# Kernel optimization log

Measured on AMD Instinct MI355X. Metric: run time of the kernel, lower is better.

The kernel has to match this reference:

```python
import jax, jax.numpy as jnp
import numpy as np
from jax import lax

# Per-tensor power-of-two scales (ScalingImplType.CONST / POWER_OF_TWO in Brevitas)
S_ACT8 = 2.0 ** -4   # 8-bit signed input quant scale
S_ACT4 = 2.0 ** -1   # 4-bit signed input quant scale
S_W = 2.0 ** -2      # per-tensor weight quant scale
S_RELU = 2.0 ** -2   # 4-bit unsigned QuantReLU scale


def fq(x, scale, qmin, qmax):
    # fake-quant with straight-through estimator (STE)
    q = jnp.clip(jnp.round(x / scale), qmin, qmax) * scale
    return x + lax.stop_gradient(q - x)


def fq_signed(x, scale, bits):
    return fq(x, scale, -(2 ** (bits - 1)), 2 ** (bits - 1) - 1)


def fq_uint(x, scale, bits):
    return fq(x, scale, 0, 2 ** bits - 1)


def qconv(x, w, in_bits, w_bits, s_in, stride=1, padding=0, groups=1):
    xq = fq_signed(x, s_in, in_bits)
    wq = fq_signed(w, S_W, w_bits)
    return lax.conv_general_dilated(
        xq, wq, (stride, stride), [(padding, padding)] * 2,
        feature_group_count=groups,
        dimension_numbers=('NCHW', 'OIHW', 'NCHW'))


def maxpool(x, k, s):
    return lax.reduce_window(x, -jnp.inf, lax.max,
                             (1, 1, k, k), (1, 1, s, s), 'VALID')


def dwsep(x, dw, pw):
    c = x.shape[1]
    x = qconv(x, dw, 4, 4, S_ACT4, padding=1, groups=c)  # depthwise 3x3
    x = qconv(x, pw, 4, 4, S_ACT4)                       # pointwise 1x1
    return x


def qrelu4(x):
    return fq_uint(jax.nn.relu(x), S_RELU, 4)


def setup_inputs() -> dict:
    key = jax.random.key(0)
    ks = jax.random.split(key, 10)
    B = 1024
    mk = lambda k, shp, sc=0.5: jax.random.normal(k, shp, jnp.float32) * sc
    return {
        'x': jax.random.normal(ks[0], (B, 3, 32, 32), jnp.float32),
        'w0': mk(ks[1], (3, 3, 1, 1)),
        'dw1': mk(ks[2], (3, 1, 3, 3)),
        'pw1': mk(ks[3], (32, 3, 1, 1)),
        'dw2': mk(ks[4], (32, 1, 3, 3)),
        'pw2': mk(ks[5], (64, 32, 1, 1)),
        'dw3': mk(ks[6], (64, 1, 3, 3)),
        'pw3': mk(ks[7], (128, 64, 1, 1)),
        'wc1': mk(ks[8], (256, 128, 1, 1)),
        'wc2': mk(ks[9], (10, 256, 1, 1)),
    }


def reference(x, w0, dw1, pw1, dw2, pw2, dw3, pw3, wc1, wc2):
    # features
    h = qconv(x, w0, 8, 8, S_ACT8)            # 1x1, 3->3, 8-bit
    h = dwsep(h, dw1, pw1)                    # 3->32, 32x32
    h = qrelu4(h)
    h = maxpool(h, 2, 2)                      # 16x16
    h = dwsep(h, dw2, pw2)                    # 32->64
    h = qrelu4(h)
    h = maxpool(h, 2, 2)                      # 8x8
    h = dwsep(h, dw3, pw3)                    # 64->128
    h = qrelu4(h)
    h = maxpool(h, 8, 1)                      # 1x1
    # classifier
    h = qconv(h, wc1, 4, 4, S_ACT4)           # 128->256
    h = qrelu4(h)
    h = qconv(h, wc2, 4, 4, S_ACT4)           # 256->10
    h = fq_signed(h, S_ACT8, 8)               # output quant int8
    return h
```

## Files before the change

kernel.cpp:

```cpp
#include <hip/hip_runtime.h>

typedef int v4i __attribute__((ext_vector_type(4)));

#define W0i   0
#define DW1i  9
#define PW1i  36
#define DW2i  132
#define DW3i  420
#define PW2p  996
#define PW3p  1508
#define WC1p  3556
#define WC2p  11748
#define PW2Fb 12388
#define PW3Fb 12900
#define DW2pk 14948
#define DW3pk 15092
#define WTOT  15380

__device__ __forceinline__ int iclamp(int v, int lo, int hi) {
  return v < lo ? lo : (v > hi ? hi : v);
}
__device__ __forceinline__ int rne4(int a) {
  return (a + 1 + ((a >> 2) & 1)) >> 2;
}
__device__ __forceinline__ int rne32(int a) {
  return (a + 15 + ((a >> 5) & 1)) >> 5;
}

__device__ __forceinline__ int dot4(int a, int b, int c) {
#if defined(__has_builtin) && __has_builtin(__builtin_amdgcn_sdot4)
  return __builtin_amdgcn_sdot4(a, b, c, false);
#else
  c += ((a << 24) >> 24) * ((b << 24) >> 24);
  c += ((a << 16) >> 24) * ((b << 16) >> 24);
  c += ((a <<  8) >> 24) * ((b <<  8) >> 24);
  c += (a >> 24) * (b >> 24);
  return c;
#endif
}

__device__ __forceinline__ int alignb(int hi, int lo, int sh) {
#if defined(__has_builtin) && __has_builtin(__builtin_amdgcn_alignbyte)
  return __builtin_amdgcn_alignbyte(hi, lo, sh);
#else
  return (int)(((((unsigned long long)(unsigned)hi) << 32) |
                (unsigned)lo) >> (8 * sh));
#endif
}

__device__ __forceinline__ int pack3(int a, int b, int c) {
  return (a & 0xff) | ((b & 0xff) << 8) | ((c & 0xff) << 16);
}

__device__ __forceinline__ int pk_mad16(int a, int b, int c) {
  int d;
  asm("v_pk_mad_i16 %0, %1, %2, %3" : "=v"(d) : "v"(a), "v"(b), "v"(c));
  return d;
}
__device__ __forceinline__ int pk_add16(int a, int b) {
  int d;
  asm("v_pk_add_i16 %0, %1, %2" : "=v"(d) : "v"(a), "v"(b));
  return d;
}
__device__ __forceinline__ int pk_ashr16(int sh, int a) {
  int d;
  asm("v_pk_ashrrev_i16 %0, %1, %2" : "=v"(d) : "v"(sh), "v"(a));
  return d;
}
__device__ __forceinline__ int pk_max16(int a, int b) {
  int d;
  asm("v_pk_max_i16 %0, %1, %2" : "=v"(d) : "v"(a), "v"(b));
  return d;
}
__device__ __forceinline__ int pk_min16(int a, int b) {
  int d;
  asm("v_pk_min_i16 %0, %1, %2" : "=v"(d) : "v"(a), "v"(b));
  return d;
}
__device__ __forceinline__ int rne4s_pk(int a) {
  const int sh = 0x00020002, one = 0x00010001;
  int t = pk_ashr16(sh, a);
  t &= one;
  t += one;
  int s4 = pk_add16(a, t);
  int r = pk_ashr16(sh, s4);
  r = pk_max16(r, (int)0xFFF8FFF8);
  r = pk_min16(r, 0x00070007);
  return r;
}

__device__ __forceinline__ int max4(v4i d) {
  int a = d[0] > d[1] ? d[0] : d[1];
  int b = d[2] > d[3] ? d[2] : d[3];
  return a > b ? a : b;
}

__global__ __launch_bounds__(256) void prep_weights(
    const float* __restrict__ w0,  const float* __restrict__ dw1,
    const float* __restrict__ pw1, const float* __restrict__ dw2,
    const float* __restrict__ pw2, const float* __restrict__ dw3,
    const float* __restrict__ pw3, const float* __restrict__ wc1,
    const float* __restrict__ wc2, int* __restrict__ ws) {
  int t = blockIdx.x * blockDim.x + threadIdx.x;
  if (t >= WTOT) return;
  if (t < PW2p) {
    float w; int lo = -8, hi = 7;
    if (t < DW1i)      { w = w0[t];        lo = -128; hi = 127; }
    else if (t < PW1i)   w = dw1[t - DW1i];
    else if (t < DW2i)   w = pw1[t - PW1i];
    else if (t < DW3i)   w = dw2[t - DW2i];
    else                 w = dw3[t - DW3i];
    ws[t] = iclamp((int)rintf(w * 4.f), lo, hi);
  } else if (t < PW2Fb) {
    const float* src;
    if (t < WC1p) {
      if (t < PW3p) src = pw2 + (t - PW2p) * 4;
      else          src = pw3 + (t - PW3p) * 4;
    } else {
      if (t < WC2p) src = wc1 + (t - WC1p) * 4;
      else          src = wc2 + (t - WC2p) * 4;
    }
    int p = 0;
#pragma unroll
    for (int b = 0; b < 4; b++) {
      int c = iclamp((int)rintf(src[b] * 4.f), -8, 7);
      p |= (c & 0xff) << (8 * b);
    }
    ws[t] = p;
  } else if (t < PW3Fb) {
    int i = t - PW2Fb;
    int nt = i >> 7, r = i & 127, lane = r >> 1, dw = r & 1;
    int n = nt * 16 + (lane & 15);
    int kb = (lane >> 4) * 8 + dw * 4;
    int p = 0;
#pragma unroll
    for (int b = 0; b < 4; b++) {
      int c = iclamp((int)rintf(pw2[n * 32 + kb + b] * 4.f), -8, 7);
      p |= (c & 0xff) << (8 * b);
    }
    ws[t] = p;
  } else if (t < DW2pk) {
    int i = t - PW3Fb;
    int g = i >> 7, r = i & 127, lane = r >> 1, dw = r & 1;
    int nt = g >> 1, kh = g & 1;
    int n = nt * 16 + (lane & 15);
    int kb = kh * 32 + (lane >> 4) * 8 + dw * 4;
    int p = 0;
#pragma unroll
    for (int b = 0; b < 4; b++) {
      int c = iclamp((int)rintf(pw3[n * 64 + kb + b] * 4.f), -8, 7);
      p |= (c & 0xff) << (8 * b);
    }
    ws[t] = p;
  } else if (t < DW3pk) {
    int i = t - DW2pk;
    int cq = i / 18, r = i - cq * 18, t9 = r >> 1, par = r & 1;
    int wl = iclamp((int)rintf(dw2[(cq * 4 + par) * 9 + t9] * 4.f), -8, 7);
    int wh = iclamp((int)rintf(dw2[(cq * 4 + 2 + par) * 9 + t9] * 4.f), -8, 7);
    ws[t] = (wl & 0xFFFF) | (wh << 16);
  } else {
    int i = t - DW3pk;
    int cq = i / 18, r = i - cq * 18, t9 = r >> 1, par = r & 1;
    int wl = iclamp((int)rintf(dw3[(cq * 4 + par) * 9 + t9] * 4.f), -8, 7);
    int wh = iclamp((int)rintf(dw3[(cq * 4 + 2 + par) * 9 + t9] * 4.f), -8, 7);
    ws[t] = (wl & 0xFFFF) | (wh << 16);
  }
}

__global__ __launch_bounds__(256, 4) void fused_net(
    const float* __restrict__ x,
    const int*   __restrict__ wq,
    float* __restrict__ out)
{
  const int img = blockIdx.x;
  const int tid = threadIdx.x;

  __shared__ __align__(16) int bufAi[2560];
  __shared__ __align__(16) int bufBi[2592];
  __shared__ int s_red[256];

  {
    const float* xim = x + (size_t)img * 3072;
    const int p4 = tid * 4;
    float4 v0 = *(const float4*)(xim + p4);
    float4 v1 = *(const float4*)(xim + 1024 + p4);
    float4 v2 = *(const float4*)(xim + 2048 + p4);
    int w[9];
#pragma unroll
    for (int i = 0; i < 9; i++) w[i] = wq[W0i + i];
#define Q8(v) iclamp((int)rintf((v) * 16.f), -128, 127)
    int a0[4] = {Q8(v0.x), Q8(v0.y), Q8(v0.z), Q8(v0.w)};
    int a1[4] = {Q8(v1.x), Q8(v1.y), Q8(v1.z), Q8(v1.w)};
    int a2[4] = {Q8(v2.x), Q8(v2.y), Q8(v2.z), Q8(v2.w)};
#undef Q8
#pragma unroll
    for (int o = 0; o < 3; o++) {
      int pk = 0;
#pragma unroll
      for (int j = 0; j < 4; j++) {
        int s = a0[j] * w[o * 3] + a1[j] * w[o * 3 + 1] + a2[j] * w[o * 3 + 2];
        pk |= (iclamp(rne32(s), -8, 7) & 0xff) << (8 * j);
      }
      bufAi[o * 256 + tid] = pk;
    }
  }
  __syncthreads();

  {
    const int y = tid >> 3, q = tid & 7;
#pragma unroll
    for (int c = 0; c < 3; c++) {
      int wr[3];
#pragma unroll
      for (int r = 0; r < 3; r++)
        wr[r] = pack3(wq[DW1i + c * 9 + r * 3], wq[DW1i + c * 9 + r * 3 + 1],
                      wq[DW1i + c * 9 + r * 3 + 2]);
      const int* ap = bufAi + c * 256;
      int acc0 = 0, acc1 = 0, acc2 = 0, acc3 = 0;
#pragma unroll
      for (int ky = 0; ky < 3; ky++) {
        int yy = y + ky - 1;
        if (yy < 0 || yy > 31) continue;
        int base = yy * 8 + q;
        int dC = ap[base];
        int dL = q ? ap[base - 1] : 0;
        int dR = (q < 7) ? ap[base + 1] : 0;
        int w = wr[ky];
        acc0 = dot4(alignb(dC, dL, 3), w, acc0);
        acc1 = dot4(dC, w, acc1);
        acc2 = dot4(alignb(dR, dC, 1), w, acc2);
        acc3 = dot4(alignb(dR, dC, 2), w, acc3);
      }
      int pk = (iclamp(rne4(acc0), -8, 7) & 0xff) |
               ((iclamp(rne4(acc1), -8, 7) & 0xff) << 8) |
               ((iclamp(rne4(acc2), -8, 7) & 0xff) << 16) |
               ((iclamp(rne4(acc3), -8, 7) & 0xff) << 24);
      bufBi[c * 256 + tid] = pk;
    }
  }
  __syncthreads();

  {
    const int py = tid >> 4, px = tid & 15;
    const unsigned char* bB = (const unsigned char*)bufBi;
    unsigned u[3][2];
#pragma unroll
    for (int c = 0; c < 3; c++)
#pragma unroll
      for (int dy = 0; dy < 2; dy++)
        u[c][dy] = *(const unsigned short*)(bB + c * 1024 +
                                            (2 * py + dy) * 32 + 2 * px);
    int a[4];
#pragma unroll
    for (int d = 0; d < 4; d++) {
      int dy = d >> 1, dx = d & 1;
      unsigned t1 = __builtin_amdgcn_perm(u[1][dy], u[0][dy],
                                          0x0C0C0000u | ((4 + dx) << 8) | dx);
      a[d] = (int)__builtin_amdgcn_perm(u[2][dy], t1,
                                        0x0C000100u | ((4 + dx) << 16));
    }
#pragma unroll
    for (int it = 0; it < 8; it++) {
      int pk = 0;
#pragma unroll
      for (int j = 0; j < 4; j++) {
        int o = it * 4 + j;
        int wpk = pack3(wq[PW1i + o * 3], wq[PW1i + o * 3 + 1],
                        wq[PW1i + o * 3 + 2]);
        int m0 = dot4(a[0], wpk, 0), m1 = dot4(a[1], wpk, 0);
        int m2 = dot4(a[2], wpk, 0), m3 = dot4(a[3], wpk, 0);
        int mx = max(max(m0, m1), max(m2, m3));
        pk |= iclamp(rne4(mx), 0, 7) << (8 * j);
      }
      bufAi[py * 149 + px * 9 + it] = pk;
    }
  }
  __syncthreads();

  for (int it2 = 0; it2 < 2; it2++) {
    int idx = tid + 256 * it2;
    int cq = __builtin_amdgcn_readfirstlane(idx >> 6);
    int s = idx & 63;
    int y = s >> 2, x0 = (s & 3) << 2;
    int we[9], wo[9];
    {
      const int2* wp = (const int2*)(wq + DW2pk + cq * 18);
#pragma unroll
      for (int t9 = 0; t9 < 9; t9++) { int2 v = wp[t9]; we[t9] = v.x; wo[t9] = v.y; }
    }
    int acce[4] = {}, acco[4] = {};
#pragma unroll
    for (int ky = 0; ky < 3; ky++) {
      int yy = y + ky - 1;
      if (yy < 0 || yy > 15) continue;
      int rb = yy * 149 + cq;
      int rd[6];
      rd[0] = (x0 > 0) ? bufAi[rb + (x0 - 1) * 9] : 0;
      rd[1] = bufAi[rb + x0 * 9];
      rd[2] = bufAi[rb + (x0 + 1) * 9];
      rd[3] = bufAi[rb + (x0 + 2) * 9];
      rd[4] = bufAi[rb + (x0 + 3) * 9];
      rd[5] = (x0 < 12) ? bufAi[rb + (x0 + 4) * 9] : 0;
      int ee[6], eo[6];
#pragma unroll
      for (int k = 0; k < 6; k++) {
        ee[k] = rd[k] & 0x000F000F;
        eo[k] = (rd[k] >> 8) & 0x000F000F;
      }
#pragma unroll
      for (int j = 0; j < 4; j++)
#pragma unroll
        for (int kx = 0; kx < 3; kx++) {
          acce[j] = pk_mad16(ee[j + kx], we[ky * 3 + kx], acce[j]);
          acco[j] = pk_mad16(eo[j + kx], wo[ky * 3 + kx], acco[j]);
        }
    }
#pragma unroll
    for (int j = 0; j < 4; j++) {
      int re = rne4s_pk(acce[j]);
      int ro = rne4s_pk(acco[j]);
      bufBi[y * 162 + (x0 + j) * 10 + cq] =
          (re & 0x00FF00FF) | ((ro & 0x00FF00FF) << 8);
    }
  }
  __syncthreads();

#pragma unroll
  for (int i = 0; i < 4; i++) {
    int id = tid + 256 * i;
    int m = id >> 2, c2 = id & 3;
    int qp = m >> 2, d = m & 3;
    int sy = ((qp >> 3) << 1) + (d >> 1);
    int sx = ((qp & 7) << 1) + (d & 1);
    long v = *(const long*)(bufBi + sy * 162 + sx * 10 + c2 * 2);
    *(long*)(bufAi + m * 10 + c2 * 2) = v;
  }
  __syncthreads();

  {
    const int w = tid >> 6, lane = tid & 63;
    const int lm = lane & 15, kg = lane >> 4;
    const int ntp = (w & 1) * 2;
    const int mtb = (w >> 1) * 8;
    const long bw0 = *(const long*)(wq + PW2Fb + (ntp * 64 + lane) * 2);
    const long bw1 = *(const long*)(wq + PW2Fb + ((ntp + 1) * 64 + lane) * 2);
    const signed char* Ab = (const signed char*)bufAi;
    signed char* A2c = (signed char*)bufBi;
    const int n0 = ntp * 16 + lm, n1 = (ntp + 1) * 16 + lm;
#pragma unroll 4
    for (int mt = mtb; mt < mtb + 8; mt++) {
      int m = mt * 16 + lm;
      long av = *(const long*)(Ab + m * 40 + kg * 8);
      v4i d0 = __builtin_amdgcn_mfma_i32_16x16x32_i8(av, bw0, (v4i){0, 0, 0, 0},
                                                     0, 0, 0);
      v4i d1 = __builtin_amdgcn_mfma_i32_16x16x32_i8(av, bw1, (v4i){0, 0, 0, 0},
                                                     0, 0, 0);
      int qp = mt * 4 + kg;
      int py = qp >> 3, px = qp & 7;
      int bb = (py * 137 + px * 17) * 4;
      A2c[bb + n0] = (signed char)iclamp(rne4(max4(d0)), 0, 7);
      A2c[bb + n1] = (signed char)iclamp(rne4(max4(d1)), 0, 7);
    }
  }
  __syncthreads();

  {
    int cq2 = tid >> 4;
    int s = tid & 15;
    int y = s >> 1, x0 = (s & 1) << 2;
    int we[9], wo[9];
    {
      const int2* wp = (const int2*)(wq + DW3pk + cq2 * 18);
#pragma unroll
      for (int t9 = 0; t9 < 9; t9++) { int2 v = wp[t9]; we[t9] = v.x; wo[t9] = v.y; }
    }
    int acce[4] = {}, acco[4] = {};
#pragma unroll
    for (int ky = 0; ky < 3; ky++) {
      int yy = y + ky - 1;
      if (yy < 0 || yy > 7) continue;
      int rb = yy * 137 + cq2;
      int rd[6];
      rd[0] = (x0 == 4) ? bufBi[rb + (x0 - 1) * 17] : 0;
      rd[1] = bufBi[rb + x0 * 17];
      rd[2] = bufBi[rb + (x0 + 1) * 17];
      rd[3] = bufBi[rb + (x0 + 2) * 17];
      rd[4] = bufBi[rb + (x0 + 3) * 17];
      rd[5] = (x0 == 0) ? bufBi[rb + (x0 + 4) * 17] : 0;
      int ee[6], eo[6];
#pragma unroll
      for (int k = 0; k < 6; k++) {
        ee[k] = rd[k] & 0x000F000F;
        eo[k] = (rd[k] >> 8) & 0x000F000F;
      }
#pragma unroll
      for (int j = 0; j < 4; j++)
#pragma unroll
        for (int kx = 0; kx < 3; kx++) {
          acce[j] = pk_mad16(ee[j + kx], we[ky * 3 + kx], acce[j]);
          acco[j] = pk_mad16(eo[j + kx], wo[ky * 3 + kx], acco[j]);
        }
    }
#pragma unroll
    for (int j = 0; j < 4; j++) {
      int re = rne4s_pk(acce[j]);
      int ro = rne4s_pk(acco[j]);
      bufAi[(y * 8 + x0 + j) * 18 + cq2] =
          (re & 0x00FF00FF) | ((ro & 0x00FF00FF) << 8);
    }
  }
  __syncthreads();

  {
    const int w = tid >> 6, lane = tid & 63;
    const int lm = lane & 15, kg = lane >> 4;
    const signed char* Ab = (const signed char*)bufAi;
    signed char* fcin = (signed char*)bufBi;
    long b0v[2], b1v[2];
#pragma unroll
    for (int h = 0; h < 2; h++) {
      int nt = w * 2 + h;
      b0v[h] = *(const long*)(wq + PW3Fb + (nt * 2 + 0) * 128 + lane * 2);
      b1v[h] = *(const long*)(wq + PW3Fb + (nt * 2 + 1) * 128 + lane * 2);
    }
    int mx[2] = {-1000000, -1000000};
#pragma unroll
    for (int mt = 0; mt < 4; mt++) {
      int m = mt * 16 + lm;
      long a0 = *(const long*)(Ab + m * 72 + kg * 8);
      long a1 = *(const long*)(Ab + m * 72 + 32 + kg * 8);
#pragma unroll
      for (int h = 0; h < 2; h++) {
        v4i d = __builtin_amdgcn_mfma_i32_16x16x32_i8(a0, b0v[h],
                                                      (v4i){0, 0, 0, 0}, 0, 0, 0);
        d = __builtin_amdgcn_mfma_i32_16x16x32_i8(a1, b1v[h], d, 0, 0, 0);
        int t4 = max4(d);
        mx[h] = mx[h] > t4 ? mx[h] : t4;
      }
    }
#pragma unroll
    for (int h = 0; h < 2; h++) {
      int red = max(mx[h], __shfl_xor(mx[h], 16));
      red = max(red, __shfl_xor(red, 32));
      if (lane < 16)
        fcin[(w * 2 + h) * 16 + lm] = (signed char)iclamp(rne4(red), 0, 7);
    }
  }
  __syncthreads();

  {
    const int4* wp = (const int4*)(wq + WC1p + tid * 32);
    const int4* mp = (const int4*)bufBi;
    int acc = 0;
#pragma unroll
    for (int rI = 0; rI < 8; rI++) {
      int4 a = mp[rI]; int4 w = wp[rI];
      acc = dot4(a.x, w.x, acc); acc = dot4(a.y, w.y, acc);
      acc = dot4(a.z, w.z, acc); acc = dot4(a.w, w.w, acc);
    }
    ((signed char*)bufAi)[tid] = (signed char)iclamp(rne4(acc), 0, 7);
  }
  __syncthreads();

  if (tid < 80) {
    int k = tid >> 3, j = tid & 7;
    const int4* wp = (const int4*)(wq + WC2p + k * 64 + j * 8);
    int4 w0v = wp[0], w1v = wp[1];
    const int4* ap = (const int4*)bufAi;
    int4 A0 = ap[j * 2], A1 = ap[j * 2 + 1];
    int acc = dot4(A0.x, w0v.x, 0);
    acc = dot4(A0.y, w0v.y, acc); acc = dot4(A0.z, w0v.z, acc);
    acc = dot4(A0.w, w0v.w, acc);
    acc = dot4(A1.x, w1v.x, acc); acc = dot4(A1.y, w1v.y, acc);
    acc = dot4(A1.z, w1v.z, acc); acc = dot4(A1.w, w1v.w, acc);
    s_red[tid] = acc;
  }
  __syncthreads();
  if (tid < 10) {
    int acc = 0;
#pragma unroll
    for (int j = 0; j < 8; j++) acc += s_red[tid * 8 + j];
    int code = iclamp(2 * acc, -128, 127);
    out[(size_t)img * 10 + tid] = (float)code * 0.0625f;
  }
}

extern "C" void kernel_launch(void* const* d_in, const int* in_sizes, int n_in,
                              void* d_out, int out_size, void* d_ws, size_t ws_size,
                              hipStream_t stream) {
  const float* x   = (const float*)d_in[0];
  const float* w0  = (const float*)d_in[1];
  const float* dw1 = (const float*)d_in[2];
  const float* pw1 = (const float*)d_in[3];
  const float* dw2 = (const float*)d_in[4];
  const float* pw2 = (const float*)d_in[5];
  const float* dw3 = (const float*)d_in[6];
  const float* pw3 = (const float*)d_in[7];
  const float* wc1 = (const float*)d_in[8];
  const float* wc2 = (const float*)d_in[9];
  int*   wsq = (int*)d_ws;
  float* out = (float*)d_out;

  prep_weights<<<(WTOT + 255) / 256, 256, 0, stream>>>(
      w0, dw1, pw1, dw2, pw2, dw3, pw3, wc1, wc2, wsq);
  fused_net<<<1024, 256, 0, stream>>>(x, wsq, out);
}
```

Baseline: 95.97 us.

## Double block size to 512 threads and redistribute per-stage work

Raises the fused per-image kernel from 256 to 512 threads and splits every stage's work across the larger block: two pixels per thread at the input, finer task splits for the depthwise and pointwise stages, and one MFMA tile per wave for pw2/pw3. It also drops the separate repack pass after the second depthwise conv by writing directly into the swizzled layout the MFMA stage reads, which removes one barrier and one LDS copy. The aim is more parallel work per image and fewer serial loop steps. The cost is higher register pressure from the 512-thread launch bounds and idle threads in the small classifier stages.

```diff
diff --git a/kernel.cpp b/kernel.cpp
--- a/kernel.cpp
+++ b/kernel.cpp
@@ -167,7 +167,7 @@
   }
 }
 
-__global__ __launch_bounds__(256, 4) void fused_net(
+__global__ __launch_bounds__(512, 8) void fused_net(
     const float* __restrict__ x,
     const int*   __restrict__ wq,
     float* __restrict__ out)
@@ -181,67 +181,65 @@
 
   {
     const float* xim = x + (size_t)img * 3072;
-    const int p4 = tid * 4;
-    float4 v0 = *(const float4*)(xim + p4);
-    float4 v1 = *(const float4*)(xim + 1024 + p4);
-    float4 v2 = *(const float4*)(xim + 2048 + p4);
+    const int p2 = tid * 2;
+    float2 v0 = *(const float2*)(xim + p2);
+    float2 v1 = *(const float2*)(xim + 1024 + p2);
+    float2 v2 = *(const float2*)(xim + 2048 + p2);
     int w[9];
 #pragma unroll
     for (int i = 0; i < 9; i++) w[i] = wq[W0i + i];
 #define Q8(v) iclamp((int)rintf((v) * 16.f), -128, 127)
-    int a0[4] = {Q8(v0.x), Q8(v0.y), Q8(v0.z), Q8(v0.w)};
-    int a1[4] = {Q8(v1.x), Q8(v1.y), Q8(v1.z), Q8(v1.w)};
-    int a2[4] = {Q8(v2.x), Q8(v2.y), Q8(v2.z), Q8(v2.w)};
+    int a0[2] = {Q8(v0.x), Q8(v0.y)};
+    int a1[2] = {Q8(v1.x), Q8(v1.y)};
+    int a2[2] = {Q8(v2.x), Q8(v2.y)};
 #undef Q8
 #pragma unroll
     for (int o = 0; o < 3; o++) {
-      int pk = 0;
-#pragma unroll
-      for (int j = 0; j < 4; j++) {
-        int s = a0[j] * w[o * 3] + a1[j] * w[o * 3 + 1] + a2[j] * w[o * 3 + 2];
-        pk |= (iclamp(rne32(s), -8, 7) & 0xff) << (8 * j);
-      }
-      bufAi[o * 256 + tid] = pk;
-    }
+      int c0 = iclamp(rne32(a0[0] * w[o * 3] + a1[0] * w[o * 3 + 1] +
+                            a2[0] * w[o * 3 + 2]), -8, 7);
+      int c1 = iclamp(rne32(a0[1] * w[o * 3] + a1[1] * w[o * 3 + 1] +
+                            a2[1] * w[o * 3 + 2]), -8, 7);
+      ((short*)bufAi)[o * 512 + tid] =
+          (short)((c0 & 0xff) | ((c1 & 0xff) << 8));
+    }
+  }
+  __syncthreads();
+
+  for (int task = tid; task < 768; task += 512) {
+    int c = task >> 8, pos = task & 255;
+    int y = pos >> 3, q = pos & 7;
+    int wr[3];
+#pragma unroll
+    for (int r = 0; r < 3; r++)
+      wr[r] = pack3(wq[DW1i + c * 9 + r * 3], wq[DW1i + c * 9 + r * 3 + 1],
+                    wq[DW1i + c * 9 + r * 3 + 2]);
+    const int* ap = bufAi + c * 256;
+    int acc0 = 0, acc1 = 0, acc2 = 0, acc3 = 0;
+#pragma unroll
+    for (int ky = 0; ky < 3; ky++) {
+      int yy = y + ky - 1;
+      if (yy < 0 || yy > 31) continue;
+      int base = yy * 8 + q;
+      int dC = ap[base];
+      int dL = q ? ap[base - 1] : 0;
+      int dR = (q < 7) ? ap[base + 1] : 0;
+      int w = wr[ky];
+      acc0 = dot4(alignb(dC, dL, 3), w, acc0);
+      acc1 = dot4(dC, w, acc1);
+      acc2 = dot4(alignb(dR, dC, 1), w, acc2);
+      acc3 = dot4(alignb(dR, dC, 2), w, acc3);
+    }
+    int pk = (iclamp(rne4(acc0), -8, 7) & 0xff) |
+             ((iclamp(rne4(acc1), -8, 7) & 0xff) << 8) |
+             ((iclamp(rne4(acc2), -8, 7) & 0xff) << 16) |
+             ((iclamp(rne4(acc3), -8, 7) & 0xff) << 24);
+    bufBi[c * 256 + pos] = pk;
   }
   __syncthreads();
 
   {
-    const int y = tid >> 3, q = tid & 7;
-#pragma unroll
-    for (int c = 0; c < 3; c++) {
-      int wr[3];
-#pragma unroll
-      for (int r = 0; r < 3; r++)
-        wr[r] = pack3(wq[DW1i + c * 9 + r * 3], wq[DW1i + c * 9 + r * 3 + 1],
-                      wq[DW1i + c * 9 + r * 3 + 2]);
-      const int* ap = bufAi + c * 256;
-      int acc0 = 0, acc1 = 0, acc2 = 0, acc3 = 0;
-#pragma unroll
-      for (int ky = 0; ky < 3; ky++) {
-        int yy = y + ky - 1;
-        if (yy < 0 || yy > 31) continue;
-        int base = yy * 8 + q;
-        int dC = ap[base];
-        int dL = q ? ap[base - 1] : 0;
-        int dR = (q < 7) ? ap[base + 1] : 0;
-        int w = wr[ky];
-        acc0 = dot4(alignb(dC, dL, 3), w, acc0);
-        acc1 = dot4(dC, w, acc1);
-        acc2 = dot4(alignb(dR, dC, 1), w, acc2);
-        acc3 = dot4(alignb(dR, dC, 2), w, acc3);
-      }
-      int pk = (iclamp(rne4(acc0), -8, 7) & 0xff) |
-               ((iclamp(rne4(acc1), -8, 7) & 0xff) << 8) |
-               ((iclamp(rne4(acc2), -8, 7) & 0xff) << 16) |
-               ((iclamp(rne4(acc3), -8, 7) & 0xff) << 24);
-      bufBi[c * 256 + tid] = pk;
-    }
-  }
-  __syncthreads();
-
-  {
-    const int py = tid >> 4, px = tid & 15;
+    const int p = tid >> 1, itb = (tid & 1) * 4;
+    const int py = p >> 4, px = p & 15;
     const unsigned char* bB = (const unsigned char*)bufBi;
     unsigned u[3][2];
 #pragma unroll
@@ -260,7 +258,7 @@
                                         0x0C000100u | ((4 + dx) << 16));
     }
 #pragma unroll
-    for (int it = 0; it < 8; it++) {
+    for (int it = itb; it < itb + 4; it++) {
       int pk = 0;
 #pragma unroll
       for (int j = 0; j < 4; j++) {
@@ -277,10 +275,9 @@
   }
   __syncthreads();
 
-  for (int it2 = 0; it2 < 2; it2++) {
-    int idx = tid + 256 * it2;
-    int cq = __builtin_amdgcn_readfirstlane(idx >> 6);
-    int s = idx & 63;
+  {
+    int cq = __builtin_amdgcn_readfirstlane(tid >> 6);
+    int s = tid & 63;
     int y = s >> 2, x0 = (s & 3) << 2;
     int we[9], wo[9];
     {
@@ -315,142 +312,102 @@
           acco[j] = pk_mad16(eo[j + kx], wo[ky * 3 + kx], acco[j]);
         }
     }
+    const int py = y >> 1, dy = y & 1;
 #pragma unroll
     for (int j = 0; j < 4; j++) {
+      int xx = x0 + j;
+      int qp = py * 8 + (xx >> 1);
+      int q = qp ^ (py & 3);
+      int m = q * 4 + dy * 2 + (xx & 1);
       int re = rne4s_pk(acce[j]);
       int ro = rne4s_pk(acco[j]);
-      bufBi[y * 162 + (x0 + j) * 10 + cq] =
-          (re & 0x00FF00FF) | ((ro & 0x00FF00FF) << 8);
-    }
-  }
-  __syncthreads();
-
-#pragma unroll
-  for (int i = 0; i < 4; i++) {
-    int id = tid + 256 * i;
-    int m = id >> 2, c2 = id & 3;
-    int qp = m >> 2, d = m & 3;
-    int sy = ((qp >> 3) << 1) + (d >> 1);
-    int sx = ((qp & 7) << 1) + (d & 1);
-    long v = *(const long*)(bufBi + sy * 162 + sx * 10 + c2 * 2);
-    *(long*)(bufAi + m * 10 + c2 * 2) = v;
+      bufBi[m * 10 + cq] = (re & 0x00FF00FF) | ((ro & 0x00FF00FF) << 8);
+    }
   }
   __syncthreads();
 
   {
     const int w = tid >> 6, lane = tid & 63;
     const int lm = lane & 15, kg = lane >> 4;
-    const int ntp = (w & 1) * 2;
-    const int mtb = (w >> 1) * 8;
-    const long bw0 = *(const long*)(wq + PW2Fb + (ntp * 64 + lane) * 2);
-    const long bw1 = *(const long*)(wq + PW2Fb + ((ntp + 1) * 64 + lane) * 2);
-    const signed char* Ab = (const signed char*)bufAi;
-    signed char* A2c = (signed char*)bufBi;
-    const int n0 = ntp * 16 + lm, n1 = (ntp + 1) * 16 + lm;
+    const int nt = w & 3, mtb = (w >> 2) * 8;
+    const long bw = *(const long*)(wq + PW2Fb + (nt * 64 + lane) * 2);
+    const signed char* Ab = (const signed char*)bufBi;
+    signed char* A2c = (signed char*)bufAi;
+    const int n = nt * 16 + lm;
 #pragma unroll 4
     for (int mt = mtb; mt < mtb + 8; mt++) {
       int m = mt * 16 + lm;
       long av = *(const long*)(Ab + m * 40 + kg * 8);
-      v4i d0 = __builtin_amdgcn_mfma_i32_16x16x32_i8(av, bw0, (v4i){0, 0, 0, 0},
+      v4i d0 = __builtin_amdgcn_mfma_i32_16x16x32_i8(av, bw, (v4i){0, 0, 0, 0},
                                                      0, 0, 0);
-      v4i d1 = __builtin_amdgcn_mfma_i32_16x16x32_i8(av, bw1, (v4i){0, 0, 0, 0},
-                                                     0, 0, 0);
-      int qp = mt * 4 + kg;
+      int q = mt * 4 + kg;
+      int qp = q ^ ((q >> 3) & 3);
       int py = qp >> 3, px = qp & 7;
-      int bb = (py * 137 + px * 17) * 4;
-      A2c[bb + n0] = (signed char)iclamp(rne4(max4(d0)), 0, 7);
-      A2c[bb + n1] = (signed char)iclamp(rne4(max4(d1)), 0, 7);
-    }
-  }
-  __syncthreads();
-
-  {
-    int cq2 = tid >> 4;
-    int s = tid & 15;
-    int y = s >> 1, x0 = (s & 1) << 2;
+      A2c[(py * 137 + px * 17) * 4 + n] =
+          (signed char)iclamp(rne4(max4(d0)), 0, 7);
+    }
+  }
+  __syncthreads();
+
+  for (int it = 0; it < 2; it++) {
+    int cq2 = __builtin_amdgcn_readfirstlane(tid >> 6) * 2 + it;
+    int pos = tid & 63;
+    int y = pos >> 3, xx = pos & 7;
     int we[9], wo[9];
     {
       const int2* wp = (const int2*)(wq + DW3pk + cq2 * 18);
 #pragma unroll
       for (int t9 = 0; t9 < 9; t9++) { int2 v = wp[t9]; we[t9] = v.x; wo[t9] = v.y; }
     }
-    int acce[4] = {}, acco[4] = {};
+    int acce = 0, acco = 0;
 #pragma unroll
     for (int ky = 0; ky < 3; ky++) {
       int yy = y + ky - 1;
       if (yy < 0 || yy > 7) continue;
-      int rb = yy * 137 + cq2;
-      int rd[6];
-      rd[0] = (x0 == 4) ? bufBi[rb + (x0 - 1) * 17] : 0;
-      rd[1] = bufBi[rb + x0 * 17];
-      rd[2] = bufBi[rb + (x0 + 1) * 17];
-      rd[3] = bufBi[rb + (x0 + 2) * 17];
-      rd[4] = bufBi[rb + (x0 + 3) * 17];
-      rd[5] = (x0 == 0) ? bufBi[rb + (x0 + 4) * 17] : 0;
-      int ee[6], eo[6];
-#pragma unroll
-      for (int k = 0; k < 6; k++) {
-        ee[k] = rd[k] & 0x000F000F;
-        eo[k] = (rd[k] >> 8) & 0x000F000F;
+#pragma unroll
+      for (int kx = 0; kx < 3; kx++) {
+        int x2 = xx + kx - 1;
+        if (x2 < 0 || x2 > 7) continue;
+        int rdv = bufAi[yy * 137 + x2 * 17 + cq2];
+        int ee = rdv & 0x000F000F, eo = (rdv >> 8) & 0x000F000F;
+        acce = pk_mad16(ee, we[ky * 3 + kx], acce);
+        acco = pk_mad16(eo, wo[ky * 3 + kx], acco);
       }
-#pragma unroll
-      for (int j = 0; j < 4; j++)
-#pragma unroll
-        for (int kx = 0; kx < 3; kx++) {
-          acce[j] = pk_mad16(ee[j + kx], we[ky * 3 + kx], acce[j]);
-          acco[j] = pk_mad16(eo[j + kx], wo[ky * 3 + kx], acco[j]);
-        }
-    }
-#pragma unroll
-    for (int j = 0; j < 4; j++) {
-      int re = rne4s_pk(acce[j]);
-      int ro = rne4s_pk(acco[j]);
-      bufAi[(y * 8 + x0 + j) * 18 + cq2] =
-          (re & 0x00FF00FF) | ((ro & 0x00FF00FF) << 8);
-    }
+    }
+    int re = rne4s_pk(acce), ro = rne4s_pk(acco);
+    bufBi[pos * 18 + cq2] = (re & 0x00FF00FF) | ((ro & 0x00FF00FF) << 8);
   }
   __syncthreads();
 
   {
-    const int w = tid >> 6, lane = tid & 63;
+    const int nt = tid >> 6, lane = tid & 63;
     const int lm = lane & 15, kg = lane >> 4;
-    const signed char* Ab = (const signed char*)bufAi;
-    signed char* fcin = (signed char*)bufBi;
-    long b0v[2], b1v[2];
-#pragma unroll
-    for (int h = 0; h < 2; h++) {
-      int nt = w * 2 + h;
-      b0v[h] = *(const long*)(wq + PW3Fb + (nt * 2 + 0) * 128 + lane * 2);
-      b1v[h] = *(const long*)(wq + PW3Fb + (nt * 2 + 1) * 128 + lane * 2);
-    }
-    int mx[2] = {-1000000, -1000000};
+    const signed char* Ab = (const signed char*)bufBi;
+    signed char* fcin = (signed char*)bufAi;
+    const long b0 = *(const long*)(wq + PW3Fb + (nt * 2 + 0) * 128 + lane * 2);
+    const long b1 = *(const long*)(wq + PW3Fb + (nt * 2 + 1) * 128 + lane * 2);
+    int mx = -1000000;
 #pragma unroll
     for (int mt = 0; mt < 4; mt++) {
       int m = mt * 16 + lm;
       long a0 = *(const long*)(Ab + m * 72 + kg * 8);
       long a1 = *(const long*)(Ab + m * 72 + 32 + kg * 8);
-#pragma unroll
-      for (int h = 0; h < 2; h++) {
-        v4i d = __builtin_amdgcn_mfma_i32_16x16x32_i8(a0, b0v[h],
-                                                      (v4i){0, 0, 0, 0}, 0, 0, 0);
-        d = __builtin_amdgcn_mfma_i32_16x16x32_i8(a1, b1v[h], d, 0, 0, 0);
-        int t4 = max4(d);
-        mx[h] = mx[h] > t4 ? mx[h] : t4;
-      }
-    }
-#pragma unroll
-    for (int h = 0; h < 2; h++) {
-      int red = max(mx[h], __shfl_xor(mx[h], 16));
-      red = max(red, __shfl_xor(red, 32));
-      if (lane < 16)
-        fcin[(w * 2 + h) * 16 + lm] = (signed char)iclamp(rne4(red), 0, 7);
-    }
-  }
-  __syncthreads();
-
-  {
+      v4i d = __builtin_amdgcn_mfma_i32_16x16x32_i8(a0, b0,
+                                                    (v4i){0, 0, 0, 0}, 0, 0, 0);
+      d = __builtin_amdgcn_mfma_i32_16x16x32_i8(a1, b1, d, 0, 0, 0);
+      int t4 = max4(d);
+      mx = mx > t4 ? mx : t4;
+    }
+    int red = max(mx, __shfl_xor(mx, 16));
+    red = max(red, __shfl_xor(red, 32));
+    if (lane < 16)
+      fcin[nt * 16 + lm] = (signed char)iclamp(rne4(red), 0, 7);
+  }
+  __syncthreads();
+
+  if (tid < 256) {
     const int4* wp = (const int4*)(wq + WC1p + tid * 32);
-    const int4* mp = (const int4*)bufBi;
+    const int4* mp = (const int4*)bufAi;
     int acc = 0;
 #pragma unroll
     for (int rI = 0; rI < 8; rI++) {
@@ -458,7 +415,7 @@
       acc = dot4(a.x, w.x, acc); acc = dot4(a.y, w.y, acc);
       acc = dot4(a.z, w.z, acc); acc = dot4(a.w, w.w, acc);
     }
-    ((signed char*)bufAi)[tid] = (signed char)iclamp(rne4(acc), 0, 7);
+    ((signed char*)bufBi)[tid] = (signed char)iclamp(rne4(acc), 0, 7);
   }
   __syncthreads();
 
@@ -466,7 +423,7 @@
     int k = tid >> 3, j = tid & 7;
     const int4* wp = (const int4*)(wq + WC2p + k * 64 + j * 8);
     int4 w0v = wp[0], w1v = wp[1];
-    const int4* ap = (const int4*)bufAi;
+    const int4* ap = (const int4*)bufBi;
     int4 A0 = ap[j * 2], A1 = ap[j * 2 + 1];
     int acc = dot4(A0.x, w0v.x, 0);
     acc = dot4(A0.y, w0v.y, acc); acc = dot4(A0.z, w0v.z, acc);
@@ -503,5 +460,5 @@
 
   prep_weights<<<(WTOT + 255) / 256, 256, 0, stream>>>(
       w0, dw1, pw1, dw2, pw2, dw3, pw3, wc1, wc2, wsq);
-  fused_net<<<1024, 256, 0, stream>>>(x, wsq, out);
-}
+  fused_net<<<1024, 512, 0, stream>>>(x, wsq, out);
+}
```

New measurement: 99.53 us. 1.04x slower.

## Drop LDS reshuffle pass, use lightweight barriers, hoist MFMA weights, shuffle-reduce classifier

Applied to the files above, without the earlier changes.

The depthwise-2 stage now writes its output straight into the pooled-quad swizzled layout that the pointwise-2 MFMA reads, removing a separate LDS copy pass and two block barriers. The buffers are ping-ponged to match. The __syncthreads calls become inline-asm s_waitcnt lgkmcnt(0) plus s_barrier, and the MFMA B-operand weight loads are hoisted to kernel start so their global latency overlaps the early stages. The final classifier uses 40 threads with a wave shuffle reduction instead of an LDS partial-sum array and an extra barrier. The custom barrier skips the vmcnt wait and relies on all cross-wave data going through LDS; the hoisted weights also stay live in registers across every stage.

```diff
diff --git a/kernel.cpp b/kernel.cpp
--- a/kernel.cpp
+++ b/kernel.cpp
@@ -25,6 +25,10 @@
 }
 __device__ __forceinline__ int rne32(int a) {
   return (a + 15 + ((a >> 5) & 1)) >> 5;
+}
+
+__device__ __forceinline__ void bar_lds() {
+  asm volatile("s_waitcnt lgkmcnt(0)\n\ts_barrier" ::: "memory");
 }
 
 __device__ __forceinline__ int dot4(int a, int b, int c) {
@@ -174,10 +178,22 @@
 {
   const int img = blockIdx.x;
   const int tid = threadIdx.x;
+  const int wv = tid >> 6, lane = tid & 63;
+  const int lm = lane & 15, kg = lane >> 4;
 
   __shared__ __align__(16) int bufAi[2560];
   __shared__ __align__(16) int bufBi[2592];
-  __shared__ int s_red[256];
+
+  const int ntp = (wv & 1) * 2;
+  const long bw0 = *(const long*)(wq + PW2Fb + (ntp * 64 + lane) * 2);
+  const long bw1 = *(const long*)(wq + PW2Fb + ((ntp + 1) * 64 + lane) * 2);
+  long b0v[2], b1v[2];
+#pragma unroll
+  for (int h = 0; h < 2; h++) {
+    int nt = wv * 2 + h;
+    b0v[h] = *(const long*)(wq + PW3Fb + (nt * 2 + 0) * 128 + lane * 2);
+    b1v[h] = *(const long*)(wq + PW3Fb + (nt * 2 + 1) * 128 + lane * 2);
+  }
 
   {
     const float* xim = x + (size_t)img * 3072;
@@ -204,7 +220,7 @@
       bufAi[o * 256 + tid] = pk;
     }
   }
-  __syncthreads();
+  bar_lds();
 
   {
     const int y = tid >> 3, q = tid & 7;
@@ -238,7 +254,7 @@
       bufBi[c * 256 + tid] = pk;
     }
   }
-  __syncthreads();
+  bar_lds();
 
   {
     const int py = tid >> 4, px = tid & 15;
@@ -275,7 +291,7 @@
       bufAi[py * 149 + px * 9 + it] = pk;
     }
   }
-  __syncthreads();
+  bar_lds();
 
   for (int it2 = 0; it2 < 2; it2++) {
     int idx = tid + 256 * it2;
@@ -315,37 +331,24 @@
           acco[j] = pk_mad16(eo[j + kx], wo[ky * 3 + kx], acco[j]);
         }
     }
+    const int py = y >> 1, dy = y & 1;
 #pragma unroll
     for (int j = 0; j < 4; j++) {
+      int xx = x0 + j;
+      int qp = py * 8 + (xx >> 1);
+      int q = qp ^ (py & 3);
+      int m = q * 4 + dy * 2 + (xx & 1);
       int re = rne4s_pk(acce[j]);
       int ro = rne4s_pk(acco[j]);
-      bufBi[y * 162 + (x0 + j) * 10 + cq] =
-          (re & 0x00FF00FF) | ((ro & 0x00FF00FF) << 8);
-    }
-  }
-  __syncthreads();
-
-#pragma unroll
-  for (int i = 0; i < 4; i++) {
-    int id = tid + 256 * i;
-    int m = id >> 2, c2 = id & 3;
-    int qp = m >> 2, d = m & 3;
-    int sy = ((qp >> 3) << 1) + (d >> 1);
-    int sx = ((qp & 7) << 1) + (d & 1);
-    long v = *(const long*)(bufBi + sy * 162 + sx * 10 + c2 * 2);
-    *(long*)(bufAi + m * 10 + c2 * 2) = v;
-  }
-  __syncthreads();
-
-  {
-    const int w = tid >> 6, lane = tid & 63;
-    const int lm = lane & 15, kg = lane >> 4;
-    const int ntp = (w & 1) * 2;
-    const int mtb = (w >> 1) * 8;
-    const long bw0 = *(const long*)(wq + PW2Fb + (ntp * 64 + lane) * 2);
-    const long bw1 = *(const long*)(wq + PW2Fb + ((ntp + 1) * 64 + lane) * 2);
-    const signed char* Ab = (const signed char*)bufAi;
-    signed char* A2c = (signed char*)bufBi;
+      bufBi[m * 10 + cq] = (re & 0x00FF00FF) | ((ro & 0x00FF00FF) << 8);
+    }
+  }
+  bar_lds();
+
+  {
+    const int mtb = (wv >> 1) * 8;
+    const signed char* Ab = (const signed char*)bufBi;
+    signed char* A2c = (signed char*)bufAi;
     const int n0 = ntp * 16 + lm, n1 = (ntp + 1) * 16 + lm;
 #pragma unroll 4
     for (int mt = mtb; mt < mtb + 8; mt++) {
@@ -355,14 +358,15 @@
                                                      0, 0, 0);
       v4i d1 = __builtin_amdgcn_mfma_i32_16x16x32_i8(av, bw1, (v4i){0, 0, 0, 0},
                                                      0, 0, 0);
-      int qp = mt * 4 + kg;
+      int q = mt * 4 + kg;
+      int qp = q ^ ((q >> 3) & 3);
       int py = qp >> 3, px = qp & 7;
       int bb = (py * 137 + px * 17) * 4;
       A2c[bb + n0] = (signed char)iclamp(rne4(max4(d0)), 0, 7);
       A2c[bb + n1] = (signed char)iclamp(rne4(max4(d1)), 0, 7);
     }
   }
-  __syncthreads();
+  bar_lds();
 
   {
     int cq2 = tid >> 4;
@@ -381,12 +385,12 @@
       if (yy < 0 || yy > 7) continue;
       int rb = yy * 137 + cq2;
       int rd[6];
-      rd[0] = (x0 == 4) ? bufBi[rb + (x0 - 1) * 17] : 0;
-      rd[1] = bufBi[rb + x0 * 17];
-      rd[2] = bufBi[rb + (x0 + 1) * 17];
-      rd[3] = bufBi[rb + (x0 + 2) * 17];
-      rd[4] = bufBi[rb + (x0 + 3) * 17];
-      rd[5] = (x0 == 0) ? bufBi[rb + (x0 + 4) * 17] : 0;
+      rd[0] = (x0 == 4) ? bufAi[rb + (x0 - 1) * 17] : 0;
+      rd[1] = bufAi[rb + x0 * 17];
+      rd[2] = bufAi[rb + (x0 + 1) * 17];
+      rd[3] = bufAi[rb + (x0 + 2) * 17];
+      rd[4] = bufAi[rb + (x0 + 3) * 17];
+      rd[5] = (x0 == 0) ? bufAi[rb + (x0 + 4) * 17] : 0;
       int ee[6], eo[6];
 #pragma unroll
       for (int k = 0; k < 6; k++) {
@@ -405,24 +409,15 @@
     for (int j = 0; j < 4; j++) {
       int re = rne4s_pk(acce[j]);
       int ro = rne4s_pk(acco[j]);
-      bufAi[(y * 8 + x0 + j) * 18 + cq2] =
+      bufBi[(y * 8 + x0 + j) * 18 + cq2] =
           (re & 0x00FF00FF) | ((ro & 0x00FF00FF) << 8);
     }
   }
-  __syncthreads();
-
-  {
-    const int w = tid >> 6, lane = tid & 63;
-    const int lm = lane & 15, kg = lane >> 4;
-    const signed char* Ab = (const signed char*)bufAi;
-    signed char* fcin = (signed char*)bufBi;
-    long b0v[2], b1v[2];
-#pragma unroll
-    for (int h = 0; h < 2; h++) {
-      int nt = w * 2 + h;
-      b0v[h] = *(const long*)(wq + PW3Fb + (nt * 2 + 0) * 128 + lane * 2);
-      b1v[h] = *(const long*)(wq + PW3Fb + (nt * 2 + 1) * 128 + lane * 2);
-    }
+  bar_lds();
+
+  {
+    const signed char* Ab = (const signed char*)bufBi;
+    signed char* fcin = (signed char*)bufAi;
     int mx[2] = {-1000000, -1000000};
 #pragma unroll
     for (int mt = 0; mt < 4; mt++) {
@@ -443,14 +438,14 @@
       int red = max(mx[h], __shfl_xor(mx[h], 16));
       red = max(red, __shfl_xor(red, 32));
       if (lane < 16)
-        fcin[(w * 2 + h) * 16 + lm] = (signed char)iclamp(rne4(red), 0, 7);
-    }
-  }
-  __syncthreads();
+        fcin[(wv * 2 + h) * 16 + lm] = (signed char)iclamp(rne4(red), 0, 7);
+    }
+  }
+  bar_lds();
 
   {
     const int4* wp = (const int4*)(wq + WC1p + tid * 32);
-    const int4* mp = (const int4*)bufBi;
+    const int4* mp = (const int4*)bufAi;
     int acc = 0;
 #pragma unroll
     for (int rI = 0; rI < 8; rI++) {
@@ -458,30 +453,27 @@
       acc = dot4(a.x, w.x, acc); acc = dot4(a.y, w.y, acc);
       acc = dot4(a.z, w.z, acc); acc = dot4(a.w, w.w, acc);
     }
-    ((signed char*)bufAi)[tid] = (signed char)iclamp(rne4(acc), 0, 7);
-  }
-  __syncthreads();
-
-  if (tid < 80) {
-    int k = tid >> 3, j = tid & 7;
-    const int4* wp = (const int4*)(wq + WC2p + k * 64 + j * 8);
-    int4 w0v = wp[0], w1v = wp[1];
-    const int4* ap = (const int4*)bufAi;
-    int4 A0 = ap[j * 2], A1 = ap[j * 2 + 1];
-    int acc = dot4(A0.x, w0v.x, 0);
-    acc = dot4(A0.y, w0v.y, acc); acc = dot4(A0.z, w0v.z, acc);
-    acc = dot4(A0.w, w0v.w, acc);
-    acc = dot4(A1.x, w1v.x, acc); acc = dot4(A1.y, w1v.y, acc);
-    acc = dot4(A1.z, w1v.z, acc); acc = dot4(A1.w, w1v.w, acc);
-    s_red[tid] = acc;
-  }
-  __syncthreads();
-  if (tid < 10) {
+    ((signed char*)bufBi)[tid] = (signed char)iclamp(rne4(acc), 0, 7);
+  }
+  bar_lds();
+
+  if (tid < 40) {
+    int k = tid >> 2, j = tid & 3;
+    const int4* wp = (const int4*)(wq + WC2p + k * 64 + j * 16);
+    const int4* ap = (const int4*)bufBi;
     int acc = 0;
 #pragma unroll
-    for (int j = 0; j < 8; j++) acc += s_red[tid * 8 + j];
-    int code = iclamp(2 * acc, -128, 127);
-    out[(size_t)img * 10 + tid] = (float)code * 0.0625f;
+    for (int r = 0; r < 4; r++) {
+      int4 a = ap[j * 4 + r]; int4 w = wp[r];
+      acc = dot4(a.x, w.x, acc); acc = dot4(a.y, w.y, acc);
+      acc = dot4(a.z, w.z, acc); acc = dot4(a.w, w.w, acc);
+    }
+    acc += __shfl_xor(acc, 1);
+    acc += __shfl_xor(acc, 2);
+    if (j == 0) {
+      int code = iclamp(2 * acc, -128, 127);
+      out[(size_t)img * 10 + k] = (float)code * 0.0625f;
+    }
   }
 }
 
```

Result: no change. 94.20 us (-1.8%).
